# Performance work log

Hardware: AMD Instinct MI355X
Metric: run time of the kernel (lower is better)

Reference implementation:

```python
import jax, jax.numpy as jnp
import numpy as np

N = 100000   # nodes
E = 1600000  # edges
H = 256      # hidden_channels
C_IN = 1
C_OUT = 6
B = 64       # graphs in batch


def setup_inputs() -> dict:
    key = jax.random.key(0)
    ks = jax.random.split(key, 14)
    x = jax.random.normal(ks[0], (N, C_IN), jnp.float32)
    edge_index = jax.random.randint(ks[1], (2, E), 0, N, dtype=jnp.int64)
    batch = jnp.sort(jax.random.randint(ks[2], (N,), 0, B, dtype=jnp.int64))
    svm_pred = jax.random.uniform(ks[3], (B,), jnp.float32)

    def w(k, shape, fan_in):
        return jax.random.normal(k, shape, jnp.float32) * (1.0 / np.sqrt(fan_in))

    return {
        "x": x, "edge_index": edge_index, "batch": batch, "svm_pred": svm_pred,
        "W1": w(ks[4], (C_IN, H), C_IN),  "b1": jnp.zeros((H,), jnp.float32),
        "W2": w(ks[5], (H, H), H),        "b2": jnp.zeros((H,), jnp.float32),
        "W3": w(ks[6], (H, H), H),        "b3": jnp.zeros((H,), jnp.float32),
        "Wf1": w(ks[7], (H + 1, 128), H + 1), "bf1": jnp.zeros((128,), jnp.float32),
        "Wf2": w(ks[8], (128, C_OUT), 128),   "bf2": jnp.zeros((C_OUT,), jnp.float32),
    }


def reference(x, edge_index, batch, svm_pred,
              W1, b1, W2, b2, W3, b3, Wf1, bf1, Wf2, bf2):
    # --- GCN normalization (PyG GCNConv default: add self-loops, sym norm) ---
    loops = jnp.arange(N, dtype=edge_index.dtype)
    src = jnp.concatenate([edge_index[0], loops])  # [E+N]
    dst = jnp.concatenate([edge_index[1], loops])  # [E+N]
    deg = jax.ops.segment_sum(jnp.ones_like(dst, dtype=x.dtype), dst, num_segments=N)
    dinv = deg ** -0.5  # deg >= 1 due to self-loops
    norm = dinv[src] * dinv[dst]  # [E+N]

    def gcn(h, W, b):
        hw = h @ W                                   # [N, H]
        msg = hw[src] * norm[:, None]                # gather + scale
        return jax.ops.segment_sum(msg, dst, num_segments=N) + b

    # Dropout is identity in eval mode.
    h = jax.nn.relu(gcn(x, W1, b1))
    h = jax.nn.relu(gcn(h, W2, b2))
    h = jax.nn.relu(gcn(h, W3, b3))

    # global_mean_pool over graph ids
    sums = jax.ops.segment_sum(h, batch, num_segments=B)            # [B, H]
    cnts = jax.ops.segment_sum(jnp.ones((N,), h.dtype), batch, num_segments=B)
    pooled = sums / jnp.maximum(cnts, 1.0)[:, None]

    feat = jnp.concatenate([pooled, svm_pred.reshape(-1, 1).astype(h.dtype)], axis=1)
    out = jax.nn.relu(feat @ Wf1 + bf1) @ Wf2 + bf2                 # [B, 6]
    return out
```

## Files before the change

### kernel.cpp

```cpp
#include <hip/hip_runtime.h>
#include <math.h>

#define N_NODES 100000
#define N_EDGES 1600000
#define HDIM    256
#define NGRAPH  64

#define SCAN_BLK 1024
#define SCAN_NB  ((N_NODES + SCAN_BLK - 1) / SCAN_BLK)

#define FB 64

typedef __attribute__((ext_vector_type(8))) short bf16x8;
typedef __attribute__((ext_vector_type(4))) float f32x4;
typedef __attribute__((ext_vector_type(8))) unsigned short u16x8;

__device__ __forceinline__ ushort f2b(float f) {
    union { float f; unsigned u; } x; x.f = f;
    unsigned u = x.u;
    unsigned r = u + 0x7fffu + ((u >> 16) & 1u);
    return (ushort)(r >> 16);
}
__device__ __forceinline__ float b2f(ushort h) {
    union { unsigned u; float f; } x; x.u = ((unsigned)h) << 16;
    return x.f;
}

__global__ void k_count(const int* __restrict__ ei, int* __restrict__ cnt,
                        int* __restrict__ slot) {
    int t = blockIdx.x * blockDim.x + threadIdx.x;
    int e0 = t * 16;
    if (e0 >= N_EDGES) return;
    int d[16];
#pragma unroll
    for (int j = 0; j < 16; ++j) d[j] = ei[N_EDGES + e0 + j];
    int s[16];
#pragma unroll
    for (int j = 0; j < 16; ++j) s[j] = atomicAdd(&cnt[d[j]], 1);
#pragma unroll
    for (int j = 0; j < 16; ++j) slot[e0 + j] = s[j];
}

__global__ __launch_bounds__(1024) void k_scan1(const int* __restrict__ cnt,
                                                int* __restrict__ rowptr,
                                                int* __restrict__ bsum) {
    __shared__ int lds[SCAN_BLK];
    int t = threadIdx.x;
    int i = blockIdx.x * SCAN_BLK + t;
    int v = (i < N_NODES) ? cnt[i] : 0;
    lds[t] = v;
    __syncthreads();
    for (int off = 1; off < SCAN_BLK; off <<= 1) {
        int u = (t >= off) ? lds[t - off] : 0;
        __syncthreads();
        lds[t] += u;
        __syncthreads();
    }
    if (i < N_NODES) rowptr[i] = lds[t] - v;
    if (t == SCAN_BLK - 1) bsum[blockIdx.x] = lds[t];
}

__global__ __launch_bounds__(128) void k_scan2(int* __restrict__ bsum) {
    __shared__ int lds[128];
    int t = threadIdx.x;
    int v = (t < SCAN_NB) ? bsum[t] : 0;
    lds[t] = v;
    __syncthreads();
    for (int off = 1; off < 128; off <<= 1) {
        int u = (t >= off) ? lds[t - off] : 0;
        __syncthreads();
        lds[t] += u;
        __syncthreads();
    }
    if (t < SCAN_NB) bsum[t] = lds[t] - v;
}

__global__ void k_dinv_fix(const int* __restrict__ cnt, const float* __restrict__ x,
                           const int* __restrict__ bsum,
                           float* __restrict__ dinv, float* __restrict__ xd,
                           int* __restrict__ rowptr) {
    int i = blockIdx.x * blockDim.x + threadIdx.x;
    if (i < N_NODES) {
        rowptr[i] += bsum[i >> 10];
        float d = (float)(cnt[i] + 1);
        float dv = 1.0f / sqrtf(d);
        dinv[i] = dv;
        xd[i] = x[i] * dv;
        if (i == 0) rowptr[N_NODES] = N_EDGES;
    }
}

__global__ void k_fill(const int* __restrict__ ei, const int* __restrict__ rowptr,
                       const int* __restrict__ slot, int* __restrict__ colv) {
    int t = blockIdx.x * blockDim.x + threadIdx.x;
    int e0 = t * 8;
    if (e0 >= N_EDGES) return;
    int d[8], sl[8], sr[8];
#pragma unroll
    for (int j = 0; j < 8; ++j) {
        d[j] = ei[N_EDGES + e0 + j];
        sl[j] = slot[e0 + j];
        sr[j] = ei[e0 + j];
    }
    int rp[8];
#pragma unroll
    for (int j = 0; j < 8; ++j) rp[j] = rowptr[d[j]];
#pragma unroll
    for (int j = 0; j < 8; ++j) colv[rp[j] + sl[j]] = sr[j];
}

__global__ __launch_bounds__(256) void k_s(const int* __restrict__ rowptr,
                                           const int* __restrict__ colv,
                                           const float* __restrict__ xd,
                                           const float* __restrict__ dinv,
                                           float2* __restrict__ sd) {
    int wid = threadIdx.x >> 6, lane = threadIdx.x & 63;
    int node = blockIdx.x * 4 + wid;
    if (node >= N_NODES) return;
    int s = rowptr[node], e = rowptr[node + 1];
    float acc = 0.f;
    for (int idx = s + lane; idx < e; idx += 64) acc += xd[colv[idx]];
#pragma unroll
    for (int off = 32; off; off >>= 1) acc += __shfl_xor(acc, off);
    if (lane == 0) {
        float dv = dinv[node];
        sd[node] = make_float2(dv * (acc + xd[node]), dv);
    }
}

__global__ __launch_bounds__(256) void k_aggM(const int* __restrict__ rowptr,
                                              const int* __restrict__ colv,
                                              const float2* __restrict__ sd,
                                              const float* __restrict__ W1,
                                              const float* __restrict__ b1,
                                              ushort* __restrict__ M) {
    int wid = threadIdx.x >> 6, lane = threadIdx.x & 63;
    int node = blockIdx.x * 4 + wid;
    if (node >= N_NODES) return;
    int c4 = lane * 4;
    float4 w = *(const float4*)&W1[c4];
    float4 b = *(const float4*)&b1[c4];
    float2 self = sd[node];
    float a0 = self.y * fmaxf(fmaf(self.x, w.x, b.x), 0.f);
    float a1 = self.y * fmaxf(fmaf(self.x, w.y, b.y), 0.f);
    float a2 = self.y * fmaxf(fmaf(self.x, w.z, b.z), 0.f);
    float a3 = self.y * fmaxf(fmaf(self.x, w.w, b.w), 0.f);
    int s = rowptr[node], e = rowptr[node + 1];
    for (int base = s; base < e; base += 64) {
        int idx = base + lane;
        float2 p = make_float2(0.f, 0.f);
        if (idx < e) p = sd[colv[idx]];
        int rem = min(64, e - base);
        int k = 0;
        for (; k + 4 <= rem; k += 4) {
            float ps0 = __shfl(p.x, k),     pd0 = __shfl(p.y, k);
            float ps1 = __shfl(p.x, k + 1), pd1 = __shfl(p.y, k + 1);
            float ps2 = __shfl(p.x, k + 2), pd2 = __shfl(p.y, k + 2);
            float ps3 = __shfl(p.x, k + 3), pd3 = __shfl(p.y, k + 3);
            a0 += pd0 * fmaxf(fmaf(ps0, w.x, b.x), 0.f)
                + pd1 * fmaxf(fmaf(ps1, w.x, b.x), 0.f)
                + pd2 * fmaxf(fmaf(ps2, w.x, b.x), 0.f)
                + pd3 * fmaxf(fmaf(ps3, w.x, b.x), 0.f);
            a1 += pd0 * fmaxf(fmaf(ps0, w.y, b.y), 0.f)
                + pd1 * fmaxf(fmaf(ps1, w.y, b.y), 0.f)
                + pd2 * fmaxf(fmaf(ps2, w.y, b.y), 0.f)
                + pd3 * fmaxf(fmaf(ps3, w.y, b.y), 0.f);
            a2 += pd0 * fmaxf(fmaf(ps0, w.z, b.z), 0.f)
                + pd1 * fmaxf(fmaf(ps1, w.z, b.z), 0.f)
                + pd2 * fmaxf(fmaf(ps2, w.z, b.z), 0.f)
                + pd3 * fmaxf(fmaf(ps3, w.z, b.z), 0.f);
            a3 += pd0 * fmaxf(fmaf(ps0, w.w, b.w), 0.f)
                + pd1 * fmaxf(fmaf(ps1, w.w, b.w), 0.f)
                + pd2 * fmaxf(fmaf(ps2, w.w, b.w), 0.f)
                + pd3 * fmaxf(fmaf(ps3, w.w, b.w), 0.f);
        }
        for (; k < rem; ++k) {
            float ps = __shfl(p.x, k);
            float pd = __shfl(p.y, k);
            a0 += pd * fmaxf(fmaf(ps, w.x, b.x), 0.f);
            a1 += pd * fmaxf(fmaf(ps, w.y, b.y), 0.f);
            a2 += pd * fmaxf(fmaf(ps, w.z, b.z), 0.f);
            a3 += pd * fmaxf(fmaf(ps, w.w, b.w), 0.f);
        }
    }
    float dvi = self.y;
    ushort4 o;
    o.x = f2b(a0 * dvi);
    o.y = f2b(a1 * dvi);
    o.z = f2b(a2 * dvi);
    o.w = f2b(a3 * dvi);
    *(ushort4*)&M[(size_t)node * HDIM + c4] = o;
}

__global__ __launch_bounds__(256) void k_packW2(const float* __restrict__ Wa,
                                                ushort* __restrict__ Wpa,
                                                const float* __restrict__ Wb,
                                                ushort* __restrict__ Wpb) {
    int bid = blockIdx.x;
    const float* W = (bid < 32) ? Wa : Wb;
    ushort* Wp = (bid < 32) ? Wpa : Wpb;
    int t = (bid & 31) * 256 + threadIdx.x;
    int lane = t & 63;
    int nt = (t >> 6) & 15;
    int k0 = t >> 10;
    int col = nt * 16 + (lane & 15);
    int kb = k0 * 32 + (lane >> 4) * 8;
    ushort o[8];
#pragma unroll
    for (int j = 0; j < 8; ++j) o[j] = f2b(W[(size_t)(kb + j) * HDIM + col]);
    *(ushort4*)&Wp[(size_t)t * 8 + 0] = make_ushort4(o[0], o[1], o[2], o[3]);
    *(ushort4*)&Wp[(size_t)t * 8 + 4] = make_ushort4(o[4], o[5], o[6], o[7]);
}

__global__ __launch_bounds__(256) void k_g23(
    const ushort* __restrict__ M,
    const ushort* __restrict__ Wp2, const float* __restrict__ b2,
    const ushort* __restrict__ Wp3, const float* __restrict__ dinv,
    ushort* __restrict__ C) {
    __shared__ __align__(16) ushort lds[FB * 256];
    char* ldsb = (char*)lds;
    int tid = threadIdx.x;
    int wave = tid >> 6, lane = tid & 63;
    int l = wave * 16 + (lane & 15);
    int node = blockIdx.x * FB + l;
    int kgrp = lane >> 4;
    bool ok = node < N_NODES;
    unsigned swz = ((unsigned)(l & 7)) << 4;
    unsigned rowb = (unsigned)l * 512;

    f32x4 acc[16];
#pragma unroll
    for (int nt = 0; nt < 16; ++nt) acc[nt] = (f32x4){0.f, 0.f, 0.f, 0.f};
    const ushort* ap = M + (size_t)(ok ? node : 0) * HDIM + kgrp * 8;
#pragma unroll 1
    for (int k0 = 0; k0 < 8; ++k0) {
        bf16x8 bf = *(const bf16x8*)(ap + k0 * 32);
        if (!ok) bf = (bf16x8){0, 0, 0, 0, 0, 0, 0, 0};
        const ushort* wp = Wp2 + ((size_t)k0 * 1024 + lane) * 8;
#pragma unroll
        for (int nt = 0; nt < 16; ++nt) {
            bf16x8 a = *(const bf16x8*)(wp + (size_t)nt * 512);
            acc[nt] = __builtin_amdgcn_mfma_f32_16x16x32_bf16(a, bf, acc[nt], 0, 0, 0);
        }
    }

#pragma unroll
    for (int nt = 0; nt < 16; ++nt) {
        int f = nt * 16 + kgrp * 4;
        float4 bv = *(const float4*)&b2[f];
        uint2 pk;
        pk.x = (unsigned)f2b(fmaxf(acc[nt][0] + bv.x, 0.f)) |
               ((unsigned)f2b(fmaxf(acc[nt][1] + bv.y, 0.f)) << 16);
        pk.y = (unsigned)f2b(fmaxf(acc[nt][2] + bv.z, 0.f)) |
               ((unsigned)f2b(fmaxf(acc[nt][3] + bv.w, 0.f)) << 16);
        *(uint2*)(ldsb + rowb + (((unsigned)(f * 2)) ^ swz)) = pk;
    }
    __syncthreads();

#pragma unroll
    for (int nt = 0; nt < 16; ++nt) acc[nt] = (f32x4){0.f, 0.f, 0.f, 0.f};
#pragma unroll 1
    for (int k0 = 0; k0 < 8; ++k0) {
        bf16x8 bf = *(const bf16x8*)(ldsb + rowb + (((unsigned)(16 * kgrp + 64 * k0)) ^ swz));
        const ushort* wp = Wp3 + ((size_t)k0 * 1024 + lane) * 8;
#pragma unroll
        for (int nt = 0; nt < 16; ++nt) {
            bf16x8 a = *(const bf16x8*)(wp + (size_t)nt * 512);
            acc[nt] = __builtin_amdgcn_mfma_f32_16x16x32_bf16(a, bf, acc[nt], 0, 0, 0);
        }
    }
    if (ok) {
        float dv = dinv[node];
        size_t base = (size_t)node * HDIM + kgrp * 4;
#pragma unroll
        for (int nt = 0; nt < 16; ++nt) {
            ushort4 o;
            o.x = f2b(acc[nt][0] * dv);
            o.y = f2b(acc[nt][1] * dv);
            o.z = f2b(acc[nt][2] * dv);
            o.w = f2b(acc[nt][3] * dv);
            *(ushort4*)&C[base + nt * 16] = o;
        }
    }
}

__global__ __launch_bounds__(1024) void k_agg_pool(
    const ushort* __restrict__ g, const int* __restrict__ rowptr,
    const int* __restrict__ colv, const float* __restrict__ dinv,
    const float* __restrict__ bias, const int* __restrict__ batch,
    float* __restrict__ pooled) {
    __shared__ float srow[16][256];
    __shared__ int wbid[16];
    int wid = threadIdx.x >> 6, lane = threadIdx.x & 63;
    int node = blockIdx.x * 16 + wid;
    bool ok = node < N_NODES;
    int nd = ok ? node : N_NODES - 1;
    int half = lane >> 5;
    int l32 = lane & 31;
    int c8 = l32 * 8;
    float acc[8];
    if (half == 0) {
        u16x8 v = *(const u16x8*)&g[(size_t)nd * HDIM + c8];
#pragma unroll
        for (int j = 0; j < 8; ++j) acc[j] = b2f(v[j]);
    } else {
#pragma unroll
        for (int j = 0; j < 8; ++j) acc[j] = 0.f;
    }
    int s = rowptr[nd], e = rowptr[nd + 1];
    int i = s;
    for (; i + 8 <= e; i += 8) {
        int base = i + half * 4;
        int n0 = colv[base + 0];
        int n1 = colv[base + 1];
        int n2 = colv[base + 2];
        int n3 = colv[base + 3];
        u16x8 v0 = *(const u16x8*)&g[(size_t)n0 * HDIM + c8];
        u16x8 v1 = *(const u16x8*)&g[(size_t)n1 * HDIM + c8];
        u16x8 v2 = *(const u16x8*)&g[(size_t)n2 * HDIM + c8];
        u16x8 v3 = *(const u16x8*)&g[(size_t)n3 * HDIM + c8];
#pragma unroll
        for (int j = 0; j < 8; ++j)
            acc[j] += (b2f(v0[j]) + b2f(v1[j])) + (b2f(v2[j]) + b2f(v3[j]));
    }
    if (i + 4 <= e) {
        int base = i + half * 2;
        int n0 = colv[base + 0];
        int n1 = colv[base + 1];
        u16x8 v0 = *(const u16x8*)&g[(size_t)n0 * HDIM + c8];
        u16x8 v1 = *(const u16x8*)&g[(size_t)n1 * HDIM + c8];
#pragma unroll
        for (int j = 0; j < 8; ++j) acc[j] += b2f(v0[j]) + b2f(v1[j]);
        i += 4;
    }
    if (i + 2 <= e) {
        int n = colv[i + half];
        u16x8 v = *(const u16x8*)&g[(size_t)n * HDIM + c8];
#pragma unroll
        for (int j = 0; j < 8; ++j) acc[j] += b2f(v[j]);
        i += 2;
    }
    if (i < e && half == 0) {
        int n = colv[i];
        u16x8 v = *(const u16x8*)&g[(size_t)n * HDIM + c8];
#pragma unroll
        for (int j = 0; j < 8; ++j) acc[j] += b2f(v[j]);
    }
#pragma unroll
    for (int j = 0; j < 8; ++j) acc[j] += __shfl_xor(acc[j], 32);
    if (half == 0) {
        float dv = dinv[nd];
        float4 bl = *(const float4*)&bias[c8];
        float4 bh = *(const float4*)&bias[c8 + 4];
        float bj[8] = {bl.x, bl.y, bl.z, bl.w, bh.x, bh.y, bh.z, bh.w};
#pragma unroll
        for (int j = 0; j < 8; ++j) {
            float v = fmaxf(fmaf(acc[j], dv, bj[j]), 0.f);
            srow[wid][c8 + j] = ok ? v : 0.f;
        }
        if (l32 == 0) wbid[wid] = batch[nd];
    }
    __syncthreads();
    if (threadIdx.x < 256) {
        int j = threadIdx.x;
        float run = srow[0][j];
        int cur = wbid[0];
        for (int w = 1; w < 16; ++w) {
            int b = wbid[w];
            if (b != cur) {
                atomicAdd(&pooled[cur * HDIM + j], run);
                run = 0.f;
                cur = b;
            }
            run += srow[w][j];
        }
        atomicAdd(&pooled[cur * HDIM + j], run);
    }
}

__global__ __launch_bounds__(128) void k_bounds(const int* __restrict__ batch,
                                                int* __restrict__ startb,
                                                float* __restrict__ pooled) {
    int t = threadIdx.x;
    if (t <= NGRAPH) {
        int lo = 0, hi = N_NODES;
        while (lo < hi) {
            int mid = (lo + hi) >> 1;
            if (batch[mid] < t) lo = mid + 1; else hi = mid;
        }
        startb[t] = lo;
    }
    for (int i = t; i < NGRAPH * HDIM; i += 128) pooled[i] = 0.f;
}

__global__ __launch_bounds__(128) void k_mlp(const float* __restrict__ pooled,
                                             const int* __restrict__ startb,
                                             const float* __restrict__ svm,
                                             const float* __restrict__ Wf1,
                                             const float* __restrict__ bf1,
                                             const float* __restrict__ Wf2,
                                             const float* __restrict__ bf2,
                                             float* __restrict__ out) {
    __shared__ float fl[257];
    __shared__ float hl[128];
    int b = blockIdx.x;
    int j = threadIdx.x;
    float cntb = fmaxf((float)(startb[b + 1] - startb[b]), 1.0f);
    for (int k = j; k < 256; k += 128) fl[k] = pooled[b * HDIM + k] / cntb;
    if (j == 0) fl[256] = svm[b];
    __syncthreads();
    float acc = bf1[j];
    for (int k = 0; k < 257; ++k) acc = fmaf(fl[k], Wf1[k * 128 + j], acc);
    hl[j] = fmaxf(acc, 0.f);
    __syncthreads();
    if (j < 6) {
        float o = bf2[j];
        for (int k = 0; k < 128; ++k) o = fmaf(hl[k], Wf2[k * 6 + j], o);
        out[b * 6 + j] = o;
    }
}

static inline size_t al256(size_t x) { return (x + 255) & ~(size_t)255; }

extern "C" void kernel_launch(void* const* d_in, const int* in_sizes, int n_in,
                              void* d_out, int out_size, void* d_ws, size_t ws_size,
                              hipStream_t stream) {
    const float* x    = (const float*)d_in[0];
    const int*   ei   = (const int*)d_in[1];
    const int*   batch= (const int*)d_in[2];
    const float* svm  = (const float*)d_in[3];
    const float* W1   = (const float*)d_in[4];
    const float* b1   = (const float*)d_in[5];
    const float* W2   = (const float*)d_in[6];
    const float* b2   = (const float*)d_in[7];
    const float* W3   = (const float*)d_in[8];
    const float* b3   = (const float*)d_in[9];
    const float* Wf1  = (const float*)d_in[10];
    const float* bf1  = (const float*)d_in[11];
    const float* Wf2  = (const float*)d_in[12];
    const float* bf2  = (const float*)d_in[13];
    float* out = (float*)d_out;

    char* w = (char*)d_ws;
    int*    cnt    = (int*)w;    w += al256((size_t)N_NODES * 4);
    int*    rowptr = (int*)w;    w += al256((size_t)(N_NODES + 1) * 4);
    int*    slot   = (int*)w;    w += al256((size_t)N_EDGES * 4);
    int*    colv   = (int*)w;    w += al256((size_t)N_EDGES * 4);
    float*  dinv   = (float*)w;  w += al256((size_t)N_NODES * 4);
    float*  xd     = (float*)w;  w += al256((size_t)N_NODES * 4);
    float2* sd     = (float2*)w; w += al256((size_t)N_NODES * 8);
    int*    startb = (int*)w;    w += al256(65 * 4);
    int*    bsum   = (int*)w;    w += al256((size_t)SCAN_NB * 4);
    float*  pooled = (float*)w;  w += al256((size_t)NGRAPH * HDIM * 4);
    ushort* Wp2    = (ushort*)w; w += al256((size_t)8 * 16 * 64 * 8 * 2);
    ushort* Wp3    = (ushort*)w; w += al256((size_t)8 * 16 * 64 * 8 * 2);
    ushort* bigA   = (ushort*)w; w += al256((size_t)N_NODES * HDIM * 2);
    ushort* bigB   = (ushort*)w; w += al256((size_t)N_NODES * HDIM * 2);

    const int nblkN = (N_NODES + 255) / 256;
    const int nblkW = (N_NODES + 3) / 4;
    const int nblkF = (N_NODES + FB - 1) / FB;
    const int nblkP = (N_NODES + 15) / 16;

    hipMemsetAsync(cnt, 0, (size_t)N_NODES * 4, stream);
    k_count<<<(N_EDGES / 16 + 255) / 256, 256, 0, stream>>>(ei, cnt, slot);
    k_scan1<<<SCAN_NB, SCAN_BLK, 0, stream>>>(cnt, rowptr, bsum);
    k_scan2<<<1, 128, 0, stream>>>(bsum);
    k_dinv_fix<<<nblkN, 256, 0, stream>>>(cnt, x, bsum, dinv, xd, rowptr);
    k_fill<<<(N_EDGES / 8 + 255) / 256, 256, 0, stream>>>(ei, rowptr, slot, colv);

    k_packW2<<<64, 256, 0, stream>>>(W2, Wp2, W3, Wp3);

    k_s<<<nblkW, 256, 0, stream>>>(rowptr, colv, xd, dinv, sd);

    k_aggM<<<nblkW, 256, 0, stream>>>(rowptr, colv, sd, W1, b1, bigA);

    k_g23<<<nblkF, 256, 0, stream>>>(bigA, Wp2, b2, Wp3, dinv, bigB);

    k_bounds<<<1, 128, 0, stream>>>(batch, startb, pooled);

    k_agg_pool<<<nblkP, 1024, 0, stream>>>(bigB, rowptr, colv, dinv, b3, batch, pooled);

    k_mlp<<<NGRAPH, 128, 0, stream>>>(pooled, startb, svm, Wf1, bf1, Wf2, bf2, out);
}
```

Before: 413.7 us.

## Fuse first-layer scalar aggregation into CSR fill and double node tile in GEMM

The per-node scalar aggregation of layer 1, formerly a separate wave-per-node CSR pass, is folded into the CSR fill kernel as float atomicAdds into a zeroed buffer, followed by a tiny elementwise kernel. The goal is to drop one full read pass over colv and the gathers. Separately, the fused W2/W3 MFMA kernel now processes two 16-node groups per wave (FB 128), so each weight fragment load serves two MFMAs. This doubles accumulator registers and LDS use, which may reduce occupancy. The atomics also make float summation order nondeterministic.

```diff
diff --git a/kernel.cpp b/kernel.cpp
--- a/kernel.cpp
+++ b/kernel.cpp
@@ -9,7 +9,7 @@
 #define SCAN_BLK 1024
 #define SCAN_NB  ((N_NODES + SCAN_BLK - 1) / SCAN_BLK)
 
-#define FB 64
+#define FB 128
 
 typedef __attribute__((ext_vector_type(8))) short bf16x8;
 typedef __attribute__((ext_vector_type(4))) float f32x4;
@@ -91,7 +91,8 @@
 }
 
 __global__ void k_fill(const int* __restrict__ ei, const int* __restrict__ rowptr,
-                       const int* __restrict__ slot, int* __restrict__ colv) {
+                       const int* __restrict__ slot, const float* __restrict__ xd,
+                       int* __restrict__ colv, float* __restrict__ sacc) {
     int t = blockIdx.x * blockDim.x + threadIdx.x;
     int e0 = t * 8;
     if (e0 >= N_EDGES) return;
@@ -105,26 +106,21 @@
     int rp[8];
 #pragma unroll
     for (int j = 0; j < 8; ++j) rp[j] = rowptr[d[j]];
+    float xs[8];
+#pragma unroll
+    for (int j = 0; j < 8; ++j) xs[j] = xd[sr[j]];
 #pragma unroll
     for (int j = 0; j < 8; ++j) colv[rp[j] + sl[j]] = sr[j];
-}
-
-__global__ __launch_bounds__(256) void k_s(const int* __restrict__ rowptr,
-                                           const int* __restrict__ colv,
-                                           const float* __restrict__ xd,
-                                           const float* __restrict__ dinv,
-                                           float2* __restrict__ sd) {
-    int wid = threadIdx.x >> 6, lane = threadIdx.x & 63;
-    int node = blockIdx.x * 4 + wid;
-    if (node >= N_NODES) return;
-    int s = rowptr[node], e = rowptr[node + 1];
-    float acc = 0.f;
-    for (int idx = s + lane; idx < e; idx += 64) acc += xd[colv[idx]];
-#pragma unroll
-    for (int off = 32; off; off >>= 1) acc += __shfl_xor(acc, off);
-    if (lane == 0) {
-        float dv = dinv[node];
-        sd[node] = make_float2(dv * (acc + xd[node]), dv);
+#pragma unroll
+    for (int j = 0; j < 8; ++j) atomicAdd(&sacc[d[j]], xs[j]);
+}
+
+__global__ void k_sd(const float* __restrict__ sacc, const float* __restrict__ xd,
+                     const float* __restrict__ dinv, float2* __restrict__ sd) {
+    int i = blockIdx.x * blockDim.x + threadIdx.x;
+    if (i < N_NODES) {
+        float dv = dinv[i];
+        sd[i] = make_float2(dv * (sacc[i] + xd[i]), dv);
     }
 }
 
@@ -221,26 +217,36 @@
     char* ldsb = (char*)lds;
     int tid = threadIdx.x;
     int wave = tid >> 6, lane = tid & 63;
-    int l = wave * 16 + (lane & 15);
-    int node = blockIdx.x * FB + l;
+    int l0 = wave * 32 + (lane & 15);
+    int l1 = l0 + 16;
+    int node0 = blockIdx.x * FB + l0;
+    int node1 = node0 + 16;
     int kgrp = lane >> 4;
-    bool ok = node < N_NODES;
-    unsigned swz = ((unsigned)(l & 7)) << 4;
-    unsigned rowb = (unsigned)l * 512;
-
-    f32x4 acc[16];
-#pragma unroll
-    for (int nt = 0; nt < 16; ++nt) acc[nt] = (f32x4){0.f, 0.f, 0.f, 0.f};
-    const ushort* ap = M + (size_t)(ok ? node : 0) * HDIM + kgrp * 8;
+    bool ok0 = node0 < N_NODES, ok1 = node1 < N_NODES;
+    unsigned swz = ((unsigned)(l0 & 7)) << 4;
+    unsigned rowb0 = (unsigned)l0 * 512, rowb1 = (unsigned)l1 * 512;
+
+    f32x4 acc0[16], acc1[16];
+#pragma unroll
+    for (int nt = 0; nt < 16; ++nt) {
+        acc0[nt] = (f32x4){0.f, 0.f, 0.f, 0.f};
+        acc1[nt] = (f32x4){0.f, 0.f, 0.f, 0.f};
+    }
+
+    const ushort* ap0 = M + (size_t)(ok0 ? node0 : 0) * HDIM + kgrp * 8;
+    const ushort* ap1 = M + (size_t)(ok1 ? node1 : 0) * HDIM + kgrp * 8;
 #pragma unroll 1
     for (int k0 = 0; k0 < 8; ++k0) {
-        bf16x8 bf = *(const bf16x8*)(ap + k0 * 32);
-        if (!ok) bf = (bf16x8){0, 0, 0, 0, 0, 0, 0, 0};
+        bf16x8 bf0 = *(const bf16x8*)(ap0 + k0 * 32);
+        bf16x8 bf1 = *(const bf16x8*)(ap1 + k0 * 32);
+        if (!ok0) bf0 = (bf16x8){0, 0, 0, 0, 0, 0, 0, 0};
+        if (!ok1) bf1 = (bf16x8){0, 0, 0, 0, 0, 0, 0, 0};
         const ushort* wp = Wp2 + ((size_t)k0 * 1024 + lane) * 8;
 #pragma unroll
         for (int nt = 0; nt < 16; ++nt) {
             bf16x8 a = *(const bf16x8*)(wp + (size_t)nt * 512);
-            acc[nt] = __builtin_amdgcn_mfma_f32_16x16x32_bf16(a, bf, acc[nt], 0, 0, 0);
+            acc0[nt] = __builtin_amdgcn_mfma_f32_16x16x32_bf16(a, bf0, acc0[nt], 0, 0, 0);
+            acc1[nt] = __builtin_amdgcn_mfma_f32_16x16x32_bf16(a, bf1, acc1[nt], 0, 0, 0);
         }
     }
 
@@ -248,37 +254,62 @@
     for (int nt = 0; nt < 16; ++nt) {
         int f = nt * 16 + kgrp * 4;
         float4 bv = *(const float4*)&b2[f];
-        uint2 pk;
-        pk.x = (unsigned)f2b(fmaxf(acc[nt][0] + bv.x, 0.f)) |
-               ((unsigned)f2b(fmaxf(acc[nt][1] + bv.y, 0.f)) << 16);
-        pk.y = (unsigned)f2b(fmaxf(acc[nt][2] + bv.z, 0.f)) |
-               ((unsigned)f2b(fmaxf(acc[nt][3] + bv.w, 0.f)) << 16);
-        *(uint2*)(ldsb + rowb + (((unsigned)(f * 2)) ^ swz)) = pk;
+        uint2 pk0, pk1;
+        pk0.x = (unsigned)f2b(fmaxf(acc0[nt][0] + bv.x, 0.f)) |
+                ((unsigned)f2b(fmaxf(acc0[nt][1] + bv.y, 0.f)) << 16);
+        pk0.y = (unsigned)f2b(fmaxf(acc0[nt][2] + bv.z, 0.f)) |
+                ((unsigned)f2b(fmaxf(acc0[nt][3] + bv.w, 0.f)) << 16);
+        pk1.x = (unsigned)f2b(fmaxf(acc1[nt][0] + bv.x, 0.f)) |
+                ((unsigned)f2b(fmaxf(acc1[nt][1] + bv.y, 0.f)) << 16);
+        pk1.y = (unsigned)f2b(fmaxf(acc1[nt][2] + bv.z, 0.f)) |
+                ((unsigned)f2b(fmaxf(acc1[nt][3] + bv.w, 0.f)) << 16);
+        unsigned fo = ((unsigned)(f * 2)) ^ swz;
+        *(uint2*)(ldsb + rowb0 + fo) = pk0;
+        *(uint2*)(ldsb + rowb1 + fo) = pk1;
     }
     __syncthreads();
 
 #pragma unroll
-    for (int nt = 0; nt < 16; ++nt) acc[nt] = (f32x4){0.f, 0.f, 0.f, 0.f};
+    for (int nt = 0; nt < 16; ++nt) {
+        acc0[nt] = (f32x4){0.f, 0.f, 0.f, 0.f};
+        acc1[nt] = (f32x4){0.f, 0.f, 0.f, 0.f};
+    }
 #pragma unroll 1
     for (int k0 = 0; k0 < 8; ++k0) {
-        bf16x8 bf = *(const bf16x8*)(ldsb + rowb + (((unsigned)(16 * kgrp + 64 * k0)) ^ swz));
+        unsigned ko = ((unsigned)(16 * kgrp + 64 * k0)) ^ swz;
+        bf16x8 bf0 = *(const bf16x8*)(ldsb + rowb0 + ko);
+        bf16x8 bf1 = *(const bf16x8*)(ldsb + rowb1 + ko);
         const ushort* wp = Wp3 + ((size_t)k0 * 1024 + lane) * 8;
 #pragma unroll
         for (int nt = 0; nt < 16; ++nt) {
             bf16x8 a = *(const bf16x8*)(wp + (size_t)nt * 512);
-            acc[nt] = __builtin_amdgcn_mfma_f32_16x16x32_bf16(a, bf, acc[nt], 0, 0, 0);
-        }
-    }
-    if (ok) {
-        float dv = dinv[node];
-        size_t base = (size_t)node * HDIM + kgrp * 4;
+            acc0[nt] = __builtin_amdgcn_mfma_f32_16x16x32_bf16(a, bf0, acc0[nt], 0, 0, 0);
+            acc1[nt] = __builtin_amdgcn_mfma_f32_16x16x32_bf16(a, bf1, acc1[nt], 0, 0, 0);
+        }
+    }
+    if (ok0) {
+        float dv = dinv[node0];
+        size_t base = (size_t)node0 * HDIM + kgrp * 4;
 #pragma unroll
         for (int nt = 0; nt < 16; ++nt) {
             ushort4 o;
-            o.x = f2b(acc[nt][0] * dv);
-            o.y = f2b(acc[nt][1] * dv);
-            o.z = f2b(acc[nt][2] * dv);
-            o.w = f2b(acc[nt][3] * dv);
+            o.x = f2b(acc0[nt][0] * dv);
+            o.y = f2b(acc0[nt][1] * dv);
+            o.z = f2b(acc0[nt][2] * dv);
+            o.w = f2b(acc0[nt][3] * dv);
+            *(ushort4*)&C[base + nt * 16] = o;
+        }
+    }
+    if (ok1) {
+        float dv = dinv[node1];
+        size_t base = (size_t)node1 * HDIM + kgrp * 4;
+#pragma unroll
+        for (int nt = 0; nt < 16; ++nt) {
+            ushort4 o;
+            o.x = f2b(acc1[nt][0] * dv);
+            o.y = f2b(acc1[nt][1] * dv);
+            o.z = f2b(acc1[nt][2] * dv);
+            o.w = f2b(acc1[nt][3] * dv);
             *(ushort4*)&C[base + nt * 16] = o;
         }
     }
@@ -443,6 +474,7 @@
 
     char* w = (char*)d_ws;
     int*    cnt    = (int*)w;    w += al256((size_t)N_NODES * 4);
+    float*  sacc   = (float*)w;  w += al256((size_t)N_NODES * 4);
     int*    rowptr = (int*)w;    w += al256((size_t)(N_NODES + 1) * 4);
     int*    slot   = (int*)w;    w += al256((size_t)N_EDGES * 4);
     int*    colv   = (int*)w;    w += al256((size_t)N_EDGES * 4);
@@ -463,16 +495,16 @@
     const int nblkP = (N_NODES + 15) / 16;
 
     hipMemsetAsync(cnt, 0, (size_t)N_NODES * 4, stream);
+    hipMemsetAsync(sacc, 0, (size_t)N_NODES * 4, stream);
     k_count<<<(N_EDGES / 16 + 255) / 256, 256, 0, stream>>>(ei, cnt, slot);
     k_scan1<<<SCAN_NB, SCAN_BLK, 0, stream>>>(cnt, rowptr, bsum);
     k_scan2<<<1, 128, 0, stream>>>(bsum);
     k_dinv_fix<<<nblkN, 256, 0, stream>>>(cnt, x, bsum, dinv, xd, rowptr);
-    k_fill<<<(N_EDGES / 8 + 255) / 256, 256, 0, stream>>>(ei, rowptr, slot, colv);
+    k_fill<<<(N_EDGES / 8 + 255) / 256, 256, 0, stream>>>(ei, rowptr, slot, xd, colv, sacc);
+    k_sd<<<nblkN, 256, 0, stream>>>(sacc, xd, dinv, sd);
 
     k_packW2<<<64, 256, 0, stream>>>(W2, Wp2, W3, Wp3);
 
-    k_s<<<nblkW, 256, 0, stream>>>(rowptr, colv, xd, dinv, sd);
-
     k_aggM<<<nblkW, 256, 0, stream>>>(rowptr, colv, sd, W1, b1, bigA);
 
     k_g23<<<nblkF, 256, 0, stream>>>(bigA, Wp2, b2, Wp3, dinv, bigB);
```

Measured after the change: 495.8 us. +19.8%, slower.
